# Kernel tuning notes

Measured on AMD Instinct MI355X. Metric: run time of the kernel, lower is better.

## Reference

```python
import jax, jax.numpy as jnp
import numpy as np

ALPHA = 0.2  # leaky_relu negative slope


def setup_inputs() -> dict:
    key = jax.random.key(0)
    ks = jax.random.split(key, 6)
    N, E, F_IN, F_OUT, E_DIM = 50000, 800000, 256, 256, 64
    h = jax.random.normal(ks[0], (N, F_IN), dtype=jnp.float32)
    e_feat = jax.random.normal(ks[1], (E, E_DIM), dtype=jnp.float32)
    W = jax.random.normal(ks[2], (F_OUT, F_IN), dtype=jnp.float32) * (1.0 / np.sqrt(F_IN))
    A = jax.random.normal(ks[3], (1, 2 * F_OUT + E_DIM), dtype=jnp.float32) * 0.05
    src = jax.random.randint(ks[4], (E,), 0, N, dtype=jnp.int32)
    dst = jax.random.randint(ks[5], (E,), 0, N, dtype=jnp.int32)
    return {"h": h, "e_feat": e_feat, "W": W, "A": A, "src": src, "dst": dst}


def reference(h, e_feat, W, A, src, dst):
    N = h.shape[0]
    F_OUT = W.shape[0]
    # equation (1): node projection
    z = h @ W.T  # [N, F_OUT]
    z_src = z[src]  # [E, F_OUT]
    z_dst = z[dst]  # [E, F_OUT]
    # equation (2): per-edge attention logit = attn_fc([z_src, z_dst, e_feat])
    # split A to avoid materializing the [E, 2F+De] concat
    a_src, a_dst, a_e = A[0, :F_OUT], A[0, F_OUT:2 * F_OUT], A[0, 2 * F_OUT:]
    logits = z_src @ a_src + z_dst @ a_dst + e_feat @ a_e  # [E]
    e = jax.nn.leaky_relu(logits, ALPHA)
    # equations (3)&(4): segment-softmax over incoming edges per destination
    m = jax.ops.segment_max(e, dst, num_segments=N)  # [N]
    ex = jnp.exp(e - m[dst])
    denom = jax.ops.segment_sum(ex, dst, num_segments=N)  # [N]
    alpha = ex / denom[dst]  # [E]
    h_out = jax.ops.segment_sum(alpha[:, None] * z_src, dst, num_segments=N)
    return h_out
```

## Files before the change

kernel.cpp:

```cpp
#include <hip/hip_runtime.h>
#include <hip/hip_bf16.h>

#define FDIM 256
#define EDIM 64
#define LEAKY 0.2f

#define BM 128
#define BN 128
#define BK 32

typedef __attribute__((ext_vector_type(8))) short bfrag;
typedef __attribute__((ext_vector_type(4))) float f4acc;

__device__ __forceinline__ unsigned f2bf(float x){
    unsigned u = __float_as_uint(x);
    return (u + 0x7FFFu + ((u >> 16) & 1u)) >> 16;
}
__device__ __forceinline__ float bf2f(unsigned b){
    return __uint_as_float(b << 16);
}
__device__ __forceinline__ unsigned pack_hi(float x, float y, float& hx, float& hy){
    unsigned bx = f2bf(x), by = f2bf(y);
    hx = bf2f(bx); hy = bf2f(by);
    return bx | (by << 16);
}
__device__ __forceinline__ unsigned pack_lo(float rx, float ry){
    return f2bf(rx) | (f2bf(ry) << 16);
}

__global__ void k_init(int* __restrict__ counts, int N){
    int i = blockIdx.x*256 + threadIdx.x;
    if (i < N) counts[i] = 0;
}

__global__ __launch_bounds__(256, 2) void k_gemm(const float* __restrict__ h,
                                                 const float* __restrict__ W,
                                                 unsigned short* __restrict__ z16, int M){
    __shared__ uint4 smA[BM*8];
    __shared__ uint4 smB[BN*8];

    int tid = threadIdx.x;
    int m0 = blockIdx.x * BM;
    int n0 = blockIdx.y * BN;

    int wid  = tid >> 6;
    int lane = tid & 63;
    int wm = (wid >> 1) * 64;
    int wn = (wid & 1) * 64;
    int l15 = lane & 15;
    int l4  = lane >> 4;

    f4acc acc[4][4];
    #pragma unroll
    for (int i = 0; i < 4; ++i)
        #pragma unroll
        for (int j = 0; j < 4; ++j)
            acc[i][j] = (f4acc)(0.f);

    for (int kc = 0; kc < FDIM; kc += BK){
        #pragma unroll
        for (int q = 0; q < 4; ++q){
            int p = tid + q*256;
            int isB = p >= 512;
            int pp = p & 511;
            int row = pp >> 2, k8 = pp & 3;
            float4 v0, v1;
            if (isB){
                const float* g = &W[(n0 + row)*FDIM + kc + k8*8];
                v0 = *(const float4*)g; v1 = *(const float4*)(g + 4);
            } else {
                int gr = m0 + row;
                if (gr < M){
                    const float* g = &h[(size_t)gr*FDIM + kc + k8*8];
                    v0 = *(const float4*)g; v1 = *(const float4*)(g + 4);
                } else {
                    v0 = make_float4(0.f,0.f,0.f,0.f); v1 = v0;
                }
            }
            int sh = k8 ^ (row & 7);
            if (isB){
                uint4 hi; float hx, hy;
                hi.x = pack_hi(v0.x, v0.y, hx, hy);
                hi.y = pack_hi(v0.z, v0.w, hx, hy);
                hi.z = pack_hi(v1.x, v1.y, hx, hy);
                hi.w = pack_hi(v1.z, v1.w, hx, hy);
                smB[row*8 + sh] = hi;
            } else {
                uint4 hi, lo; float hx, hy;
                hi.x = pack_hi(v0.x, v0.y, hx, hy);
                lo.x = pack_lo(v0.x - hx, v0.y - hy);
                hi.y = pack_hi(v0.z, v0.w, hx, hy);
                lo.y = pack_lo(v0.z - hx, v0.w - hy);
                hi.z = pack_hi(v1.x, v1.y, hx, hy);
                lo.z = pack_lo(v1.x - hx, v1.y - hy);
                hi.w = pack_hi(v1.z, v1.w, hx, hy);
                lo.w = pack_lo(v1.z - hx, v1.w - hy);
                smA[row*8 + sh]       = hi;
                smA[row*8 + (sh ^ 4)] = lo;
            }
        }
        __syncthreads();

        bfrag ah[4], al[4];
        #pragma unroll
        for (int mf = 0; mf < 4; ++mf){
            int row = wm + mf*16 + l15;
            int sh = l4 ^ (row & 7);
            ah[mf] = *(const bfrag*)&smA[row*8 + sh];
            al[mf] = *(const bfrag*)&smA[row*8 + (sh ^ 4)];
        }
        #pragma unroll
        for (int nf = 0; nf < 4; ++nf){
            int row = wn + nf*16 + l15;
            int sh = l4 ^ (row & 7);
            bfrag bh = *(const bfrag*)&smB[row*8 + sh];
            #pragma unroll
            for (int mf = 0; mf < 4; ++mf){
                acc[mf][nf] = __builtin_amdgcn_mfma_f32_16x16x32_bf16(ah[mf], bh, acc[mf][nf], 0, 0, 0);
                acc[mf][nf] = __builtin_amdgcn_mfma_f32_16x16x32_bf16(al[mf], bh, acc[mf][nf], 0, 0, 0);
            }
        }
        __syncthreads();
    }

    #pragma unroll
    for (int mf = 0; mf < 4; ++mf){
        #pragma unroll
        for (int nf = 0; nf < 4; ++nf){
            int gcol = n0 + wn + nf*16 + l15;
            #pragma unroll
            for (int r = 0; r < 4; ++r){
                int grow = m0 + wm + mf*16 + l4*4 + r;
                if (grow < M)
                    z16[(size_t)grow*FDIM + gcol] = (unsigned short)f2bf(acc[mf][nf][r]);
            }
        }
    }
}

__global__ void k_sdots(const unsigned short* __restrict__ z16, const float* __restrict__ A,
                        float* __restrict__ s_src, float* __restrict__ s_dst, int N){
    int gt = blockIdx.x*256 + threadIdx.x;
    int w = gt >> 6, lane = gt & 63;
    if (w >= N) return;
    uint2 raw = *(const uint2*)&z16[(size_t)w*FDIM + lane*4];
    float z0 = bf2f(raw.x & 0xffffu), z1 = bf2f(raw.x >> 16);
    float z2 = bf2f(raw.y & 0xffffu), z3 = bf2f(raw.y >> 16);
    float4 as = *(const float4*)&A[lane*4];
    float4 ad = *(const float4*)&A[FDIM + lane*4];
    float vs = z0*as.x + z1*as.y + z2*as.z + z3*as.w;
    float vd = z0*ad.x + z1*ad.y + z2*ad.z + z3*ad.w;
    #pragma unroll
    for (int o = 32; o > 0; o >>= 1){
        vs += __shfl_xor(vs, o);
        vd += __shfl_xor(vd, o);
    }
    if (lane == 0){ s_src[w] = vs; s_dst[w] = vd; }
}

__global__ void k_count(const int* __restrict__ dst, int* __restrict__ counts, int E){
    int e = blockIdx.x*256 + threadIdx.x;
    if (e < E) atomicAdd(&counts[dst[e]], 1);
}

__global__ void k_chunk_sums(const int* __restrict__ counts, int* __restrict__ bsums, int N){
    __shared__ int sh[256];
    int base = blockIdx.x*1024;
    int s = 0;
    for (int i = threadIdx.x; i < 1024; i += 256){
        int idx = base + i;
        s += (idx < N) ? counts[idx] : 0;
    }
    sh[threadIdx.x] = s; __syncthreads();
    for (int o = 128; o > 0; o >>= 1){
        if (threadIdx.x < o) sh[threadIdx.x] += sh[threadIdx.x + o];
        __syncthreads();
    }
    if (threadIdx.x == 0) bsums[blockIdx.x] = sh[0];
}

__global__ void k_scan_small(int* __restrict__ b, int nb){
    __shared__ int sh[1024];
    int tid = threadIdx.x;
    int v = (tid < nb) ? b[tid] : 0;
    sh[tid] = v; __syncthreads();
    int acc = v;
    for (int o = 1; o < 1024; o <<= 1){
        int t = (tid >= o) ? sh[tid - o] : 0;
        __syncthreads();
        acc += t; sh[tid] = acc;
        __syncthreads();
    }
    if (tid < nb) b[tid] = acc - v;
}

__global__ void k_scan_chunks(int* __restrict__ counts, int* __restrict__ cursor,
                              const int* __restrict__ bsums, int N, int E){
    __shared__ int sh[256];
    int tid = threadIdx.x;
    int base = blockIdx.x*1024 + tid*4;
    int v[4]; int s = 0;
    #pragma unroll
    for (int l = 0; l < 4; l++){
        int idx = base + l;
        v[l] = (idx < N) ? counts[idx] : 0;
        s += v[l];
    }
    sh[tid] = s; __syncthreads();
    int acc = s;
    for (int o = 1; o < 256; o <<= 1){
        int t = (tid >= o) ? sh[tid - o] : 0;
        __syncthreads();
        acc += t; sh[tid] = acc;
        __syncthreads();
    }
    int excl = acc - s + bsums[blockIdx.x];
    #pragma unroll
    for (int l = 0; l < 4; l++){
        int idx = base + l;
        if (idx < N){ counts[idx] = excl; cursor[idx] = excl; }
        excl += v[l];
    }
    if (blockIdx.x == 0 && tid == 0) counts[N] = E;
}

__global__ void k_edge(const float* __restrict__ ef, const float* __restrict__ A,
                       const float* __restrict__ s_src, const float* __restrict__ s_dst,
                       const int* __restrict__ src, const int* __restrict__ dst,
                       int* __restrict__ cursor, int2* __restrict__ epair, int E){
    int gt = blockIdx.x*256 + threadIdx.x;
    int e = gt >> 4, l4 = gt & 15;
    if (e >= E) return;
    float4 f  = *(const float4*)&ef[(size_t)e*EDIM + l4*4];
    float4 ae = *(const float4*)&A[2*FDIM + l4*4];
    float v = f.x*ae.x + f.y*ae.y + f.z*ae.z + f.w*ae.w;
    v += __shfl_xor(v, 8); v += __shfl_xor(v, 4);
    v += __shfl_xor(v, 2); v += __shfl_xor(v, 1);
    if (l4 == 0){
        int d = dst[e];
        float lg = v + s_src[src[e]] + s_dst[d];
        lg = lg > 0.f ? lg : LEAKY*lg;
        int p = atomicAdd(&cursor[d], 1);
        int2 pr; pr.x = src[e]; pr.y = __float_as_int(lg);
        epair[p] = pr;
    }
}

__global__ __launch_bounds__(256) void k_out(const unsigned short* __restrict__ z16,
                                             const int* __restrict__ offsets,
                                             const int2* __restrict__ epair,
                                             float* __restrict__ out, int N){
    int n = blockIdx.x*4 + (threadIdx.x >> 6);
    int lane = threadIdx.x & 63;
    if (n >= N) return;
    int i0 = offsets[n], i1 = offsets[n+1];

    float mx = -3.402823466e38f;
    for (int i = i0; i < i1; ++i)
        mx = fmaxf(mx, __int_as_float(epair[i].y));

    float4 a0 = make_float4(0,0,0,0), a1 = a0, a2 = a0, a3 = a0;
    float ds0 = 0.f, ds1 = 0.f, ds2 = 0.f, ds3 = 0.f;
    const unsigned short* zb = z16 + lane*4;
    int i = i0;
    for (; i + 3 < i1; i += 4){
        int2 p0 = epair[i], p1 = epair[i+1], p2 = epair[i+2], p3 = epair[i+3];
        uint2 r0 = *(const uint2*)&zb[(size_t)p0.x*FDIM];
        uint2 r1 = *(const uint2*)&zb[(size_t)p1.x*FDIM];
        uint2 r2 = *(const uint2*)&zb[(size_t)p2.x*FDIM];
        uint2 r3 = *(const uint2*)&zb[(size_t)p3.x*FDIM];
        float w0 = __expf(__int_as_float(p0.y) - mx);
        float w1 = __expf(__int_as_float(p1.y) - mx);
        float w2 = __expf(__int_as_float(p2.y) - mx);
        float w3 = __expf(__int_as_float(p3.y) - mx);
        ds0 += w0; ds1 += w1; ds2 += w2; ds3 += w3;
        a0.x += w0*bf2f(r0.x & 0xffffu); a0.y += w0*bf2f(r0.x >> 16);
        a0.z += w0*bf2f(r0.y & 0xffffu); a0.w += w0*bf2f(r0.y >> 16);
        a1.x += w1*bf2f(r1.x & 0xffffu); a1.y += w1*bf2f(r1.x >> 16);
        a1.z += w1*bf2f(r1.y & 0xffffu); a1.w += w1*bf2f(r1.y >> 16);
        a2.x += w2*bf2f(r2.x & 0xffffu); a2.y += w2*bf2f(r2.x >> 16);
        a2.z += w2*bf2f(r2.y & 0xffffu); a2.w += w2*bf2f(r2.y >> 16);
        a3.x += w3*bf2f(r3.x & 0xffffu); a3.y += w3*bf2f(r3.x >> 16);
        a3.z += w3*bf2f(r3.y & 0xffffu); a3.w += w3*bf2f(r3.y >> 16);
    }
    for (; i < i1; ++i){
        int2 p0 = epair[i];
        uint2 r0 = *(const uint2*)&zb[(size_t)p0.x*FDIM];
        float w0 = __expf(__int_as_float(p0.y) - mx);
        ds0 += w0;
        a0.x += w0*bf2f(r0.x & 0xffffu); a0.y += w0*bf2f(r0.x >> 16);
        a0.z += w0*bf2f(r0.y & 0xffffu); a0.w += w0*bf2f(r0.y >> 16);
    }
    float dsum = (ds0 + ds1) + (ds2 + ds3);
    float inv = (i1 > i0) ? 1.f / dsum : 0.f;
    float4 res;
    res.x = ((a0.x + a1.x) + (a2.x + a3.x)) * inv;
    res.y = ((a0.y + a1.y) + (a2.y + a3.y)) * inv;
    res.z = ((a0.z + a1.z) + (a2.z + a3.z)) * inv;
    res.w = ((a0.w + a1.w) + (a2.w + a3.w)) * inv;
    *(float4*)&out[(size_t)n*FDIM + lane*4] = res;
}

extern "C" void kernel_launch(void* const* d_in, const int* in_sizes, int n_in,
                              void* d_out, int out_size, void* d_ws, size_t ws_size,
                              hipStream_t stream){
    const float* h  = (const float*)d_in[0];
    const float* ef = (const float*)d_in[1];
    const float* W  = (const float*)d_in[2];
    const float* A  = (const float*)d_in[3];
    const int*  src = (const int*)d_in[4];
    const int*  dst = (const int*)d_in[5];
    float* out = (float*)d_out;
    int N = in_sizes[0] / FDIM;
    int E = in_sizes[4];

    char* ws = (char*)d_ws;
    size_t off = 0;
    auto alloc = [&](size_t nbytes)->char*{
        char* p = ws + off;
        off = (off + nbytes + 255) & ~(size_t)255;
        return p;
    };
    unsigned short* z16 = (unsigned short*)alloc((size_t)N*FDIM*2);
    float* s_src  = (float*)alloc((size_t)N*4);
    float* s_dst  = (float*)alloc((size_t)N*4);
    int*   counts = (int*)alloc((size_t)(N+1)*4);
    int*   cursor = (int*)alloc((size_t)N*4);
    int2*  epair  = (int2*)alloc((size_t)E*8);
    int*   bsums  = (int*)alloc(1024*4);

    int nb = (N + 1023)/1024;

    hipLaunchKernelGGL(k_init, dim3((N+255)/256), dim3(256), 0, stream,
                       counts, N);
    hipLaunchKernelGGL(k_gemm, dim3((N+BM-1)/BM, FDIM/BN), dim3(256), 0, stream,
                       h, W, z16, N);
    hipLaunchKernelGGL(k_sdots, dim3((N+3)/4), dim3(256), 0, stream,
                       z16, A, s_src, s_dst, N);
    hipLaunchKernelGGL(k_count, dim3((E+255)/256), dim3(256), 0, stream,
                       dst, counts, E);
    hipLaunchKernelGGL(k_chunk_sums, dim3(nb), dim3(256), 0, stream,
                       counts, bsums, N);
    hipLaunchKernelGGL(k_scan_small, dim3(1), dim3(1024), 0, stream,
                       bsums, nb);
    hipLaunchKernelGGL(k_scan_chunks, dim3(nb), dim3(256), 0, stream,
                       counts, cursor, bsums, N, E);
    hipLaunchKernelGGL(k_edge, dim3((E+15)/16), dim3(256), 0, stream,
                       ef, A, s_src, s_dst, src, dst, cursor, epair, E);
    hipLaunchKernelGGL(k_out, dim3((N+3)/4), dim3(256), 0, stream,
                       z16, counts, epair, out, N);
}
```

Before: 242.2 us.

## Fuse attention dot products into GEMM epilogue and precompute segment max atomically

Computes the per-node source and destination attention dots directly from the fp32 GEMM accumulators, reduced across lanes and the two column tiles through shared memory and atomics, which removes the separate k_sdots pass over z. The per-destination max is now built with float atomic max in the edge kernel, so k_out no longer makes a first pass over its edge list to find it. The gather loop in k_out is unrolled to 8 edges to put more loads in flight. In exchange this adds atomic traffic in the edge kernel and atomics in the GEMM epilogue, and changes rounding slightly because the dots now use fp32 accumulators instead of bf16 z.

```diff
diff --git a/kernel.cpp b/kernel.cpp
--- a/kernel.cpp
+++ b/kernel.cpp
@@ -28,16 +28,30 @@
     return f2bf(rx) | (f2bf(ry) << 16);
 }
 
-__global__ void k_init(int* __restrict__ counts, int N){
+__device__ __forceinline__ void atomic_max_float(float* addr, float val){
+    if (val >= 0.f) atomicMax((int*)addr, __float_as_int(val));
+    else            atomicMin((unsigned int*)addr, (unsigned int)__float_as_int(val));
+}
+
+__global__ void k_init(float* __restrict__ m, float* __restrict__ s_src,
+                       float* __restrict__ s_dst, int* __restrict__ counts, int N){
     int i = blockIdx.x*256 + threadIdx.x;
-    if (i < N) counts[i] = 0;
+    if (i < N){
+        m[i] = -3.402823466e38f;
+        s_src[i] = 0.f; s_dst[i] = 0.f;
+        counts[i] = 0;
+    }
 }
 
 __global__ __launch_bounds__(256, 2) void k_gemm(const float* __restrict__ h,
                                                  const float* __restrict__ W,
-                                                 unsigned short* __restrict__ z16, int M){
+                                                 const float* __restrict__ A,
+                                                 unsigned short* __restrict__ z16,
+                                                 float* __restrict__ s_src,
+                                                 float* __restrict__ s_dst, int M){
     __shared__ uint4 smA[BM*8];
     __shared__ uint4 smB[BN*8];
+    __shared__ float sred[2][2][BM];
 
     int tid = threadIdx.x;
     int m0 = blockIdx.x * BM;
@@ -136,26 +150,44 @@
             }
         }
     }
-}
-
-__global__ void k_sdots(const unsigned short* __restrict__ z16, const float* __restrict__ A,
-                        float* __restrict__ s_src, float* __restrict__ s_dst, int N){
-    int gt = blockIdx.x*256 + threadIdx.x;
-    int w = gt >> 6, lane = gt & 63;
-    if (w >= N) return;
-    uint2 raw = *(const uint2*)&z16[(size_t)w*FDIM + lane*4];
-    float z0 = bf2f(raw.x & 0xffffu), z1 = bf2f(raw.x >> 16);
-    float z2 = bf2f(raw.y & 0xffffu), z3 = bf2f(raw.y >> 16);
-    float4 as = *(const float4*)&A[lane*4];
-    float4 ad = *(const float4*)&A[FDIM + lane*4];
-    float vs = z0*as.x + z1*as.y + z2*as.z + z3*as.w;
-    float vd = z0*ad.x + z1*ad.y + z2*ad.z + z3*ad.w;
-    #pragma unroll
-    for (int o = 32; o > 0; o >>= 1){
-        vs += __shfl_xor(vs, o);
-        vd += __shfl_xor(vd, o);
-    }
-    if (lane == 0){ s_src[w] = vs; s_dst[w] = vd; }
+
+    float aS[4], aD[4];
+    #pragma unroll
+    for (int nf = 0; nf < 4; ++nf){
+        int gcol = n0 + wn + nf*16 + l15;
+        aS[nf] = A[gcol];
+        aD[nf] = A[FDIM + gcol];
+    }
+    #pragma unroll
+    for (int mf = 0; mf < 4; ++mf){
+        #pragma unroll
+        for (int r = 0; r < 4; ++r){
+            float ps = 0.f, pd = 0.f;
+            #pragma unroll
+            for (int nf = 0; nf < 4; ++nf){
+                ps += acc[mf][nf][r] * aS[nf];
+                pd += acc[mf][nf][r] * aD[nf];
+            }
+            #pragma unroll
+            for (int o = 1; o < 16; o <<= 1){
+                ps += __shfl_xor(ps, o);
+                pd += __shfl_xor(pd, o);
+            }
+            if (l15 == 0){
+                int row = wm + mf*16 + l4*4 + r;
+                sred[wid & 1][0][row] = ps;
+                sred[wid & 1][1][row] = pd;
+            }
+        }
+    }
+    __syncthreads();
+    if (tid < BM){
+        int grow = m0 + tid;
+        if (grow < M){
+            atomicAdd(&s_src[grow], sred[0][0][tid] + sred[1][0][tid]);
+            atomicAdd(&s_dst[grow], sred[0][1][tid] + sred[1][1][tid]);
+        }
+    }
 }
 
 __global__ void k_count(const int* __restrict__ dst, int* __restrict__ counts, int E){
@@ -227,7 +259,8 @@
 __global__ void k_edge(const float* __restrict__ ef, const float* __restrict__ A,
                        const float* __restrict__ s_src, const float* __restrict__ s_dst,
                        const int* __restrict__ src, const int* __restrict__ dst,
-                       int* __restrict__ cursor, int2* __restrict__ epair, int E){
+                       float* __restrict__ m, int* __restrict__ cursor,
+                       int2* __restrict__ epair, int E){
     int gt = blockIdx.x*256 + threadIdx.x;
     int e = gt >> 4, l4 = gt & 15;
     if (e >= E) return;
@@ -240,6 +273,7 @@
         int d = dst[e];
         float lg = v + s_src[src[e]] + s_dst[d];
         lg = lg > 0.f ? lg : LEAKY*lg;
+        atomic_max_float(&m[d], lg);
         int p = atomicAdd(&cursor[d], 1);
         int2 pr; pr.x = src[e]; pr.y = __float_as_int(lg);
         epair[p] = pr;
@@ -249,55 +283,69 @@
 __global__ __launch_bounds__(256) void k_out(const unsigned short* __restrict__ z16,
                                              const int* __restrict__ offsets,
                                              const int2* __restrict__ epair,
+                                             const float* __restrict__ m,
                                              float* __restrict__ out, int N){
     int n = blockIdx.x*4 + (threadIdx.x >> 6);
     int lane = threadIdx.x & 63;
     if (n >= N) return;
     int i0 = offsets[n], i1 = offsets[n+1];
-
-    float mx = -3.402823466e38f;
-    for (int i = i0; i < i1; ++i)
-        mx = fmaxf(mx, __int_as_float(epair[i].y));
-
-    float4 a0 = make_float4(0,0,0,0), a1 = a0, a2 = a0, a3 = a0;
-    float ds0 = 0.f, ds1 = 0.f, ds2 = 0.f, ds3 = 0.f;
+    float mx = m[n];
+
+    float4 a[4];
+    a[0] = make_float4(0,0,0,0); a[1] = a[0]; a[2] = a[0]; a[3] = a[0];
+    float ds[4] = {0.f, 0.f, 0.f, 0.f};
     const unsigned short* zb = z16 + lane*4;
+
     int i = i0;
+    for (; i + 7 < i1; i += 8){
+        int2 p[8]; uint2 r[8];
+        #pragma unroll
+        for (int j = 0; j < 8; ++j) p[j] = epair[i+j];
+        #pragma unroll
+        for (int j = 0; j < 8; ++j) r[j] = *(const uint2*)&zb[(size_t)p[j].x*FDIM];
+        #pragma unroll
+        for (int j = 0; j < 8; ++j){
+            float w = __expf(__int_as_float(p[j].y) - mx);
+            ds[j & 3] += w;
+            a[j & 3].x += w*bf2f(r[j].x & 0xffffu);
+            a[j & 3].y += w*bf2f(r[j].x >> 16);
+            a[j & 3].z += w*bf2f(r[j].y & 0xffffu);
+            a[j & 3].w += w*bf2f(r[j].y >> 16);
+        }
+    }
     for (; i + 3 < i1; i += 4){
-        int2 p0 = epair[i], p1 = epair[i+1], p2 = epair[i+2], p3 = epair[i+3];
-        uint2 r0 = *(const uint2*)&zb[(size_t)p0.x*FDIM];
-        uint2 r1 = *(const uint2*)&zb[(size_t)p1.x*FDIM];
-        uint2 r2 = *(const uint2*)&zb[(size_t)p2.x*FDIM];
-        uint2 r3 = *(const uint2*)&zb[(size_t)p3.x*FDIM];
-        float w0 = __expf(__int_as_float(p0.y) - mx);
-        float w1 = __expf(__int_as_float(p1.y) - mx);
-        float w2 = __expf(__int_as_float(p2.y) - mx);
-        float w3 = __expf(__int_as_float(p3.y) - mx);
-        ds0 += w0; ds1 += w1; ds2 += w2; ds3 += w3;
-        a0.x += w0*bf2f(r0.x & 0xffffu); a0.y += w0*bf2f(r0.x >> 16);
-        a0.z += w0*bf2f(r0.y & 0xffffu); a0.w += w0*bf2f(r0.y >> 16);
-        a1.x += w1*bf2f(r1.x & 0xffffu); a1.y += w1*bf2f(r1.x >> 16);
-        a1.z += w1*bf2f(r1.y & 0xffffu); a1.w += w1*bf2f(r1.y >> 16);
-        a2.x += w2*bf2f(r2.x & 0xffffu); a2.y += w2*bf2f(r2.x >> 16);
-        a2.z += w2*bf2f(r2.y & 0xffffu); a2.w += w2*bf2f(r2.y >> 16);
-        a3.x += w3*bf2f(r3.x & 0xffffu); a3.y += w3*bf2f(r3.x >> 16);
-        a3.z += w3*bf2f(r3.y & 0xffffu); a3.w += w3*bf2f(r3.y >> 16);
+        int2 p[4]; uint2 r[4];
+        #pragma unroll
+        for (int j = 0; j < 4; ++j) p[j] = epair[i+j];
+        #pragma unroll
+        for (int j = 0; j < 4; ++j) r[j] = *(const uint2*)&zb[(size_t)p[j].x*FDIM];
+        #pragma unroll
+        for (int j = 0; j < 4; ++j){
+            float w = __expf(__int_as_float(p[j].y) - mx);
+            ds[j] += w;
+            a[j].x += w*bf2f(r[j].x & 0xffffu);
+            a[j].y += w*bf2f(r[j].x >> 16);
+            a[j].z += w*bf2f(r[j].y & 0xffffu);
+            a[j].w += w*bf2f(r[j].y >> 16);
+        }
     }
     for (; i < i1; ++i){
         int2 p0 = epair[i];
         uint2 r0 = *(const uint2*)&zb[(size_t)p0.x*FDIM];
-        float w0 = __expf(__int_as_float(p0.y) - mx);
-        ds0 += w0;
-        a0.x += w0*bf2f(r0.x & 0xffffu); a0.y += w0*bf2f(r0.x >> 16);
-        a0.z += w0*bf2f(r0.y & 0xffffu); a0.w += w0*bf2f(r0.y >> 16);
-    }
-    float dsum = (ds0 + ds1) + (ds2 + ds3);
+        float w = __expf(__int_as_float(p0.y) - mx);
+        ds[0] += w;
+        a[0].x += w*bf2f(r0.x & 0xffffu);
+        a[0].y += w*bf2f(r0.x >> 16);
+        a[0].z += w*bf2f(r0.y & 0xffffu);
+        a[0].w += w*bf2f(r0.y >> 16);
+    }
+    float dsum = (ds[0] + ds[1]) + (ds[2] + ds[3]);
     float inv = (i1 > i0) ? 1.f / dsum : 0.f;
     float4 res;
-    res.x = ((a0.x + a1.x) + (a2.x + a3.x)) * inv;
-    res.y = ((a0.y + a1.y) + (a2.y + a3.y)) * inv;
-    res.z = ((a0.z + a1.z) + (a2.z + a3.z)) * inv;
-    res.w = ((a0.w + a1.w) + (a2.w + a3.w)) * inv;
+    res.x = ((a[0].x + a[1].x) + (a[2].x + a[3].x)) * inv;
+    res.y = ((a[0].y + a[1].y) + (a[2].y + a[3].y)) * inv;
+    res.z = ((a[0].z + a[1].z) + (a[2].z + a[3].z)) * inv;
+    res.w = ((a[0].w + a[1].w) + (a[2].w + a[3].w)) * inv;
     *(float4*)&out[(size_t)n*FDIM + lane*4] = res;
 }
 
@@ -324,6 +372,7 @@
     unsigned short* z16 = (unsigned short*)alloc((size_t)N*FDIM*2);
     float* s_src  = (float*)alloc((size_t)N*4);
     float* s_dst  = (float*)alloc((size_t)N*4);
+    float* mbuf   = (float*)alloc((size_t)N*4);
     int*   counts = (int*)alloc((size_t)(N+1)*4);
     int*   cursor = (int*)alloc((size_t)N*4);
     int2*  epair  = (int2*)alloc((size_t)E*8);
@@ -332,11 +381,9 @@
     int nb = (N + 1023)/1024;
 
     hipLaunchKernelGGL(k_init, dim3((N+255)/256), dim3(256), 0, stream,
-                       counts, N);
+                       mbuf, s_src, s_dst, counts, N);
     hipLaunchKernelGGL(k_gemm, dim3((N+BM-1)/BM, FDIM/BN), dim3(256), 0, stream,
-                       h, W, z16, N);
-    hipLaunchKernelGGL(k_sdots, dim3((N+3)/4), dim3(256), 0, stream,
-                       z16, A, s_src, s_dst, N);
+                       h, W, A, z16, s_src, s_dst, N);
     hipLaunchKernelGGL(k_count, dim3((E+255)/256), dim3(256), 0, stream,
                        dst, counts, E);
     hipLaunchKernelGGL(k_chunk_sums, dim3(nb), dim3(256), 0, stream,
@@ -346,7 +393,7 @@
     hipLaunchKernelGGL(k_scan_chunks, dim3(nb), dim3(256), 0, stream,
                        counts, cursor, bsums, N, E);
     hipLaunchKernelGGL(k_edge, dim3((E+15)/16), dim3(256), 0, stream,
-                       ef, A, s_src, s_dst, src, dst, cursor, epair, E);
+                       ef, A, s_src, s_dst, src, dst, mbuf, cursor, epair, E);
     hipLaunchKernelGGL(k_out, dim3((N+3)/4), dim3(256), 0, stream,
-                       z16, counts, epair, out, N);
-}
+                       z16, counts, epair, mbuf, out, N);
+}
```

New measurement: 237.3 us. -2.0%, faster.
